# Kernel tuning notes

Measured on AMD Instinct MI355X. Metric: run time of the kernel, lower is better.

The kernel has to match this reference:

```python
import jax, jax.numpy as jnp
import numpy as np

EMBED_DIM = 1024
NUM_HEADS = 16
HEAD_DIM = EMBED_DIM // NUM_HEADS
CONSTANT = 1.0
EPS = 1e-4


def setup_inputs() -> dict:
    key = jax.random.key(0)
    ks = jax.random.split(key, 9)
    L, N, E = 2048, 4, EMBED_DIM
    scale = 1.0 / np.sqrt(E)
    return {
        "query": jax.random.normal(ks[0], (L, N, E), jnp.float32),
        "key": jax.random.normal(ks[1], (L, N, E), jnp.float32),
        "value": jax.random.normal(ks[2], (L, N, E), jnp.float32),
        "Wq": jax.random.normal(ks[3], (E, E), jnp.float32) * scale,
        "bq": jnp.zeros((E,), jnp.float32),
        "Wk": jax.random.normal(ks[4], (E, E), jnp.float32) * scale,
        "bk": jnp.zeros((E,), jnp.float32),
        "Wv": jax.random.normal(ks[5], (E, E), jnp.float32) * scale,
        "bv": jnp.zeros((E,), jnp.float32),
    }


def reference(query, key, value, Wq, bq, Wk, bk, Wv, bv):
    tgt_len, bsz, E = query.shape
    src_len = key.shape[0]
    h, d = NUM_HEADS, HEAD_DIM

    # Linear projections (nn.Linear: x @ W.T + b)
    q = query @ Wq.T + bq
    k = key @ Wk.T + bk
    v = value @ Wv.T + bv

    # (L, N, E) -> (N*h, L, d)
    def split_heads(x, slen):
        return x.reshape(slen, bsz * h, d).transpose(1, 0, 2)

    q = jax.nn.relu(split_heads(q, tgt_len))
    k = jax.nn.relu(split_heads(k, src_len))
    v = split_heads(v, src_len)

    # sin/cos positional reweighting: idx = pi/2 * arange(1, m+1) * constant / m
    m = max(src_len, tgt_len)
    idx = (np.pi / 2) * jnp.arange(1, m + 1, dtype=q.dtype) * CONSTANT / m  # (m,)
    sin_w = jnp.sin(idx)[None, :, None]  # (1, m, 1)
    cos_w = jnp.cos(idx)[None, :, None]

    q_ = jnp.concatenate([q * sin_w[:, :tgt_len], q * cos_w[:, :tgt_len]], axis=-1)  # (n, L, 2d)
    k_ = jnp.concatenate([k * sin_w[:, :src_len], k * cos_w[:, :src_len]], axis=-1)  # (n, S, 2d)

    # Non-causal linear attention: O(N) in sequence length
    kv_ = jnp.einsum('nld,nlm->ndm', k_, v)                       # (n, 2d, d)
    z_ = 1.0 / jnp.clip(jnp.einsum('nld,nd->nl', q_, k_.sum(axis=1)), EPS, None)  # (n, L)
    attn_output = jnp.einsum('nld,ndm,nl->nlm', q_, kv_, z_)      # (n, L, d)

    # (N*h, L, d) -> (L, N, E)
    attn_output = attn_output.transpose(1, 0, 2).reshape(tgt_len, bsz, E)
    return attn_output
```

## Files before the change

kernel.cpp:

```cpp
#include <hip/hip_runtime.h>
#include <cstdint>

#define L_SEQ 2048
#define NB 4
#define EMB 1024
#define NHEAD 16
#define HD 64
#define M_ROWS (L_SEQ * NB)
#define ANGC (1.5707963267948966f / 2048.0f)
#define NSPLIT 16
#define XN ((size_t)M_ROWS * EMB)
#define WN ((size_t)EMB * EMB)
#define NX8 (1 << 20)
#define NW8 (1 << 17)

typedef __bf16 bf16x8 __attribute__((ext_vector_type(8)));
typedef float f32x4 __attribute__((ext_vector_type(4)));
typedef unsigned short u16x8 __attribute__((ext_vector_type(8)));

__device__ __forceinline__ unsigned short f2bf(float f) {
  unsigned int u = __float_as_uint(f);
  u += 0x7fffu + ((u >> 16) & 1u);
  return (unsigned short)(u >> 16);
}
__device__ __forceinline__ float bf2f(unsigned short u) {
  return __uint_as_float((unsigned int)u << 16);
}

__device__ __forceinline__ void gload_lds16(const void* g, void* l) {
  __builtin_amdgcn_global_load_lds(
      (const __attribute__((address_space(1))) void*)g,
      (__attribute__((address_space(3))) void*)l, 16, 0, 0);
}

__global__ __launch_bounds__(256) void cvt_all_kernel(
    const float* __restrict__ q, const float* __restrict__ k,
    const float* __restrict__ v, const float* __restrict__ wq,
    const float* __restrict__ wk, const float* __restrict__ wv,
    unsigned short* __restrict__ xb, unsigned short* __restrict__ wb) {
  int i = blockIdx.x * 256 + threadIdx.x;
  const float* src;
  unsigned short* dst;
  int off;
  if (i < 3 * NX8) {
    int sel = i >> 20;
    off = i & (NX8 - 1);
    src = (sel == 0) ? q : (sel == 1) ? k : v;
    dst = xb + (size_t)sel * XN;
  } else {
    int j = i - 3 * NX8;
    int sel = j >> 17;
    off = j & (NW8 - 1);
    src = (sel == 0) ? wq : (sel == 1) ? wk : wv;
    dst = wb + (size_t)sel * WN;
  }
  const float4* s4 = (const float4*)src;
  float4 a = s4[off * 2], b = s4[off * 2 + 1];
  union { unsigned short u[8]; uint4 vv; } o;
  o.u[0] = f2bf(a.x); o.u[1] = f2bf(a.y); o.u[2] = f2bf(a.z); o.u[3] = f2bf(a.w);
  o.u[4] = f2bf(b.x); o.u[5] = f2bf(b.y); o.u[6] = f2bf(b.z); o.u[7] = f2bf(b.w);
  *(uint4*)(dst + (size_t)off * 8) = o.vv;
}

__global__ __launch_bounds__(256) void proj_gemm_kernel(
    const unsigned short* __restrict__ Xall, const unsigned short* __restrict__ Wall,
    const float* __restrict__ b0, const float* __restrict__ b1,
    const float* __restrict__ b2, unsigned short* __restrict__ Pall) {
  const int which = blockIdx.z;
  const unsigned short* Xb = Xall + (size_t)which * XN;
  const unsigned short* Wb = Wall + (size_t)which * WN;
  const float* bias = (which == 0) ? b0 : (which == 1) ? b1 : b2;
  unsigned short* outp = Pall + (size_t)which * XN;
  const bool relu = (which < 2);
  const int bm0 = blockIdx.x * 128;
  const int bn0 = blockIdx.y * 128;

  __shared__ unsigned short As[2][128 * 32];
  __shared__ unsigned short Bs[2][128 * 32];

  const int tid = threadIdx.x;
  const int lane = tid & 63, wave = tid >> 6;
  const int wrow = (wave >> 1) * 64, wcol = (wave & 1) * 64;
  const int fr = lane & 15, fk = lane >> 4;

  f32x4 acc[4][4];
#pragma unroll
  for (int m = 0; m < 4; ++m)
#pragma unroll
    for (int n = 0; n < 4; ++n) acc[m][n] = (f32x4){0.f, 0.f, 0.f, 0.f};

  auto stage = [&](int kt, int buf) {
#pragma unroll
    for (int i = 0; i < 2; ++i) {
      int c = i * 256 + wave * 64 + lane;
      int row = c >> 2;
      int kgs = (c & 3) ^ ((row >> 1) & 3);
      int ldsoff = (i * 256 + wave * 64) * 16;
      gload_lds16(Xb + (size_t)(bm0 + row) * EMB + kt * 32 + kgs * 8,
                  (char*)&As[buf][0] + ldsoff);
      gload_lds16(Wb + (size_t)(bn0 + row) * EMB + kt * 32 + kgs * 8,
                  (char*)&Bs[buf][0] + ldsoff);
    }
  };

  stage(0, 0);
  __syncthreads();
  const int NK = EMB / 32;
  for (int kt = 0; kt < NK; ++kt) {
    int buf = kt & 1;
    if (kt + 1 < NK) stage(kt + 1, buf ^ 1);
    bf16x8 af[4], bfr[4];
#pragma unroll
    for (int m = 0; m < 4; ++m) {
      int row = wrow + m * 16 + fr;
      af[m] = *(const bf16x8*)((const char*)&As[buf][0] + row * 64 +
                               ((fk ^ ((row >> 1) & 3)) * 16));
    }
#pragma unroll
    for (int n = 0; n < 4; ++n) {
      int row = wcol + n * 16 + fr;
      bfr[n] = *(const bf16x8*)((const char*)&Bs[buf][0] + row * 64 +
                                ((fk ^ ((row >> 1) & 3)) * 16));
    }
#pragma unroll
    for (int m = 0; m < 4; ++m)
#pragma unroll
      for (int n = 0; n < 4; ++n)
        acc[m][n] = __builtin_amdgcn_mfma_f32_16x16x32_bf16(af[m], bfr[n],
                                                            acc[m][n], 0, 0, 0);
    __syncthreads();
  }

#pragma unroll
  for (int n = 0; n < 4; ++n) {
    int gc = bn0 + wcol + n * 16 + fr;
    float bv = bias[gc];
#pragma unroll
    for (int m = 0; m < 4; ++m) {
#pragma unroll
      for (int r = 0; r < 4; ++r) {
        int gr = bm0 + wrow + m * 16 + fk * 4 + r;
        float v = acc[m][n][r] + bv;
        if (relu) v = fmaxf(v, 0.f);
        outp[(size_t)gr * EMB + gc] = f2bf(v);
      }
    }
  }
}

__global__ __launch_bounds__(256) void kv_part_kernel(
    const unsigned short* __restrict__ kp, const unsigned short* __restrict__ vp,
    float* __restrict__ kvpart, float* __restrict__ kspart) {
  const int n = blockIdx.y;
  const int s = blockIdx.x;
  const int nb = n >> 4, head = n & 15;
  const int l0 = s * (L_SEQ / NSPLIT);
  __shared__ float kt[32][64];
  __shared__ float vt[32][64];
  __shared__ float wt[2][32];
  const int t = threadIdx.x;
  const int dg = t >> 3, mg = t & 7;

  float acc[4][8];
#pragma unroll
  for (int a = 0; a < 4; ++a)
#pragma unroll
    for (int b = 0; b < 8; ++b) acc[a][b] = 0.f;
  float ks[4] = {0.f, 0.f, 0.f, 0.f};

  for (int lt = l0; lt < l0 + (L_SEQ / NSPLIT); lt += 32) {
    {
      int i = t >> 3, c8 = (t & 7) * 8;
      u16x8 gk8 = *(const u16x8*)(kp + (size_t)((lt + i) * NB + nb) * EMB +
                                  head * HD + c8);
      u16x8 gv8 = *(const u16x8*)(vp + (size_t)((lt + i) * NB + nb) * EMB +
                                  head * HD + c8);
      float4 ka = {bf2f(gk8[0]), bf2f(gk8[1]), bf2f(gk8[2]), bf2f(gk8[3])};
      float4 kb = {bf2f(gk8[4]), bf2f(gk8[5]), bf2f(gk8[6]), bf2f(gk8[7])};
      float4 va = {bf2f(gv8[0]), bf2f(gv8[1]), bf2f(gv8[2]), bf2f(gv8[3])};
      float4 vb = {bf2f(gv8[4]), bf2f(gv8[5]), bf2f(gv8[6]), bf2f(gv8[7])};
      *(float4*)&kt[i][c8] = ka;
      *(float4*)&kt[i][c8 + 4] = kb;
      *(float4*)&vt[i][c8] = va;
      *(float4*)&vt[i][c8 + 4] = vb;
    }
    if (t < 32) {
      float ang = ANGC * (float)(lt + t + 1);
      wt[0][t] = __sinf(ang);
      wt[1][t] = __cosf(ang);
    }
    __syncthreads();
#pragma unroll 4
    for (int i = 0; i < 32; ++i) {
      float w = wt[dg >> 4][i];
      float4 kk4 = *(const float4*)&kt[i][(dg & 15) * 4];
      float kk[4];
      kk[0] = fmaxf(kk4.x, 0.f) * w; kk[1] = fmaxf(kk4.y, 0.f) * w;
      kk[2] = fmaxf(kk4.z, 0.f) * w; kk[3] = fmaxf(kk4.w, 0.f) * w;
      float4 v0 = *(const float4*)&vt[i][mg * 8];
      float4 v1 = *(const float4*)&vt[i][mg * 8 + 4];
      float vv[8] = {v0.x, v0.y, v0.z, v0.w, v1.x, v1.y, v1.z, v1.w};
#pragma unroll
      for (int a = 0; a < 4; ++a) {
#pragma unroll
        for (int b = 0; b < 8; ++b) acc[a][b] += kk[a] * vv[b];
        ks[a] += kk[a];
      }
    }
    __syncthreads();
  }

  float* kvn = kvpart + ((size_t)(s * 64 + n) * 128 + dg * 4) * 64 + mg * 8;
#pragma unroll
  for (int a = 0; a < 4; ++a) {
    *(float4*)&kvn[(size_t)a * 64 + 0] = *(float4*)&acc[a][0];
    *(float4*)&kvn[(size_t)a * 64 + 4] = *(float4*)&acc[a][4];
  }
  if (mg == 0) {
#pragma unroll
    for (int a = 0; a < 4; ++a)
      kspart[(size_t)(s * 64 + n) * 128 + dg * 4 + a] = ks[a];
  }
}

__global__ __launch_bounds__(256) void kv_reduce_kernel(
    const float* __restrict__ kvpart, const float* __restrict__ kspart,
    float* __restrict__ kv, float* __restrict__ ksum) {
  const int b = blockIdx.x;
  const int t = threadIdx.x;
  if (b < 512) {
    int idx = b * 256 + t;
    f32x4 sum = (f32x4){0, 0, 0, 0};
#pragma unroll
    for (int p = 0; p < NSPLIT; ++p)
      sum += ((const f32x4*)kvpart)[(size_t)p * 131072 + idx];
    ((f32x4*)kv)[idx] = sum;
  } else {
#pragma unroll
    for (int j = 0; j < 8; ++j) {
      int idx = j * 256 + t;
      f32x4 sum = (f32x4){0, 0, 0, 0};
#pragma unroll
      for (int p = 0; p < NSPLIT; ++p)
        sum += ((const f32x4*)kspart)[(size_t)p * 2048 + idx];
      ((f32x4*)ksum)[idx] = sum;
    }
  }
}

__global__ __launch_bounds__(256) void out_kernel(
    const unsigned short* __restrict__ qp, const float* __restrict__ kv,
    const float* __restrict__ ksum, float* __restrict__ out) {
  const int n = blockIdx.y;
  const int nb = n >> 4, head = n & 15;
  const int L0 = blockIdx.x * 64;
  __shared__ float kvt[128][64];
  __shared__ float qt[64][68];
  __shared__ float kss[128];
  const int t = threadIdx.x;

  {
    const float4* src = (const float4*)(kv + (size_t)n * 128 * 64);
    float4* dst = (float4*)&kvt[0][0];
#pragma unroll
    for (int j = 0; j < 8; ++j) dst[j * 256 + t] = src[j * 256 + t];
    if (t < 128) kss[t] = ksum[n * 128 + t];
  }
  {
    int j = t >> 2, c16 = (t & 3) * 16;
    const unsigned short* gq =
        qp + (size_t)((L0 + j) * NB + nb) * EMB + head * HD + c16;
    u16x8 qa = *(const u16x8*)gq;
    u16x8 qb = *(const u16x8*)(gq + 8);
#pragma unroll
    for (int u = 0; u < 8; ++u) {
      qt[j][c16 + u] = fmaxf(bf2f(qa[u]), 0.f);
      qt[j][c16 + 8 + u] = fmaxf(bf2f(qb[u]), 0.f);
    }
  }
  __syncthreads();

  const int lg = t >> 4, mg = t & 15;
  float sw[4], cw[4];
#pragma unroll
  for (int a = 0; a < 4; ++a) {
    float ang = ANGC * (float)(L0 + lg * 4 + a + 1);
    sw[a] = __sinf(ang);
    cw[a] = __cosf(ang);
  }

  f32x4 accs[4], accc[4];
  float dns[4] = {0, 0, 0, 0}, dnc[4] = {0, 0, 0, 0};
#pragma unroll
  for (int a = 0; a < 4; ++a) {
    accs[a] = (f32x4){0, 0, 0, 0};
    accc[a] = (f32x4){0, 0, 0, 0};
  }

#pragma unroll 4
  for (int c = 0; c < 64; ++c) {
    f32x4 kvs = *(const f32x4*)&kvt[c][mg * 4];
    f32x4 kvc = *(const f32x4*)&kvt[64 + c][mg * 4];
    float kssv = kss[c], kscv = kss[64 + c];
#pragma unroll
    for (int a = 0; a < 4; ++a) {
      float qv = qt[lg * 4 + a][c];
      accs[a] += qv * kvs;
      accc[a] += qv * kvc;
      dns[a] += qv * kssv;
      dnc[a] += qv * kscv;
    }
  }

#pragma unroll
  for (int a = 0; a < 4; ++a) {
    float den = sw[a] * dns[a] + cw[a] * dnc[a];
    float z = 1.f / fmaxf(den, 1e-4f);
    int l = L0 + lg * 4 + a;
    f32x4 o = (sw[a] * accs[a] + cw[a] * accc[a]) * z;
    *(f32x4*)&out[((size_t)l * NB + nb) * EMB + head * HD + mg * 4] = o;
  }
}

extern "C" void kernel_launch(void* const* d_in, const int* in_sizes, int n_in,
                              void* d_out, int out_size, void* d_ws, size_t ws_size,
                              hipStream_t stream) {
  const float* query = (const float*)d_in[0];
  const float* key = (const float*)d_in[1];
  const float* value = (const float*)d_in[2];
  const float* Wq = (const float*)d_in[3];
  const float* bq = (const float*)d_in[4];
  const float* Wk = (const float*)d_in[5];
  const float* bk = (const float*)d_in[6];
  const float* Wv = (const float*)d_in[7];
  const float* bv = (const float*)d_in[8];
  float* out = (float*)d_out;

  char* ws = (char*)d_ws;
  const size_t need = 3 * XN * 2 + 3 * WN * 2 + 3 * XN * 2 +
                      (size_t)(64 * 128 * 64 + 64 * 128) * 4;
  if (ws_size < need) return;

  unsigned short* xb = (unsigned short*)ws;
  unsigned short* wb = (unsigned short*)(ws + 3 * XN * 2);
  unsigned short* proj = (unsigned short*)(ws + 3 * XN * 2 + 3 * WN * 2);
  float* kvb = (float*)(ws + 3 * XN * 2 + 3 * WN * 2 + 3 * XN * 2);
  float* ksb = kvb + 64 * 128 * 64;
  float* kvpart = (float*)ws;
  float* kspart = (float*)(ws + (size_t)NSPLIT * 64 * 128 * 64 * 4);

  const int total8 = 3 * NX8 + 3 * NW8;
  cvt_all_kernel<<<total8 / 256, 256, 0, stream>>>(query, key, value, Wq, Wk, Wv,
                                                   xb, wb);
  proj_gemm_kernel<<<dim3(64, 8, 3), 256, 0, stream>>>(xb, wb, bq, bk, bv, proj);
  kv_part_kernel<<<dim3(NSPLIT, 64), 256, 0, stream>>>(proj + 1 * XN, proj + 2 * XN,
                                                       kvpart, kspart);
  kv_reduce_kernel<<<513, 256, 0, stream>>>(kvpart, kspart, kvb, ksb);
  out_kernel<<<dim3(32, 64), 256, 0, stream>>>(proj, kvb, ksb, out);
}
```

Baseline: 344.2 us.

## Compute attention output with bf16 MFMA and emit transposed bf16 KV from reduce

The output stage now folds the sin/cos weights into a bf16 copy of q in LDS and runs the q·kv product on MFMA 16x16x32 bf16 instructions in place of scalar fp32 FMAs. The normaliser is computed separately from LDS. The reduce kernel now makes one block per head, sums the partial kv results, and writes kv transposed as bf16 to suit the MFMA B operand. The projection GEMM is split into three templated launches, one per matrix, with the branch on which matrix is selected at compile time. Rounding q·sin/cos and kv to bf16 lowers accuracy, the reduce step now runs on only 64 blocks, and the three separate GEMM launches add launch overhead.

```diff
diff --git a/kernel.cpp b/kernel.cpp
--- a/kernel.cpp
+++ b/kernel.cpp
@@ -62,16 +62,14 @@
   *(uint4*)(dst + (size_t)off * 8) = o.vv;
 }
 
+template <int WHICH>
 __global__ __launch_bounds__(256) void proj_gemm_kernel(
     const unsigned short* __restrict__ Xall, const unsigned short* __restrict__ Wall,
-    const float* __restrict__ b0, const float* __restrict__ b1,
-    const float* __restrict__ b2, unsigned short* __restrict__ Pall) {
-  const int which = blockIdx.z;
-  const unsigned short* Xb = Xall + (size_t)which * XN;
-  const unsigned short* Wb = Wall + (size_t)which * WN;
-  const float* bias = (which == 0) ? b0 : (which == 1) ? b1 : b2;
-  unsigned short* outp = Pall + (size_t)which * XN;
-  const bool relu = (which < 2);
+    const float* __restrict__ bias, unsigned short* __restrict__ Pall) {
+  const unsigned short* Xb = Xall + (size_t)WHICH * XN;
+  const unsigned short* Wb = Wall + (size_t)WHICH * WN;
+  unsigned short* outp = Pall + (size_t)WHICH * XN;
+  const bool relu = (WHICH < 2);
   const int bm0 = blockIdx.x * 128;
   const int bn0 = blockIdx.y * 128;
 
@@ -225,100 +223,135 @@
 
 __global__ __launch_bounds__(256) void kv_reduce_kernel(
     const float* __restrict__ kvpart, const float* __restrict__ kspart,
-    float* __restrict__ kv, float* __restrict__ ksum) {
-  const int b = blockIdx.x;
+    unsigned short* __restrict__ kvT, float* __restrict__ ksum) {
+  const int n = blockIdx.x;
   const int t = threadIdx.x;
-  if (b < 512) {
-    int idx = b * 256 + t;
-    f32x4 sum = (f32x4){0, 0, 0, 0};
+  __shared__ float kvsum[128][65];
+
+#pragma unroll
+  for (int j = 0; j < 8; ++j) {
+    int f4 = j * 256 + t;
+    int dd = f4 >> 4, m4 = f4 & 15;
+    f32x4 s = (f32x4){0, 0, 0, 0};
 #pragma unroll
     for (int p = 0; p < NSPLIT; ++p)
-      sum += ((const f32x4*)kvpart)[(size_t)p * 131072 + idx];
-    ((f32x4*)kv)[idx] = sum;
-  } else {
-#pragma unroll
-    for (int j = 0; j < 8; ++j) {
-      int idx = j * 256 + t;
-      f32x4 sum = (f32x4){0, 0, 0, 0};
-#pragma unroll
-      for (int p = 0; p < NSPLIT; ++p)
-        sum += ((const f32x4*)kspart)[(size_t)p * 2048 + idx];
-      ((f32x4*)ksum)[idx] = sum;
-    }
-  }
-}
-
-__global__ __launch_bounds__(256) void out_kernel(
-    const unsigned short* __restrict__ qp, const float* __restrict__ kv,
+      s += *(const f32x4*)(kvpart + (((size_t)(p * 64 + n) * 128 + dd) * 64) +
+                           m4 * 4);
+    kvsum[dd][m4 * 4 + 0] = s[0];
+    kvsum[dd][m4 * 4 + 1] = s[1];
+    kvsum[dd][m4 * 4 + 2] = s[2];
+    kvsum[dd][m4 * 4 + 3] = s[3];
+  }
+  if (t < 128) {
+    float s = 0.f;
+#pragma unroll
+    for (int p = 0; p < NSPLIT; ++p) s += kspart[(size_t)(p * 64 + n) * 128 + t];
+    ksum[n * 128 + t] = s;
+  }
+  __syncthreads();
+
+  int m = t >> 2, dseg = t & 3;
+#pragma unroll
+  for (int gg = 0; gg < 4; ++gg) {
+    int dd0 = dseg * 32 + gg * 8;
+    union { unsigned short u[8]; uint4 vv; } o;
+#pragma unroll
+    for (int e = 0; e < 8; ++e) o.u[e] = f2bf(kvsum[dd0 + e][m]);
+    *(uint4*)(kvT + ((size_t)n * 64 + m) * 128 + dd0) = o.vv;
+  }
+}
+
+__global__ __launch_bounds__(256) void out_mfma_kernel(
+    const unsigned short* __restrict__ qp, const unsigned short* __restrict__ kvT,
     const float* __restrict__ ksum, float* __restrict__ out) {
   const int n = blockIdx.y;
   const int nb = n >> 4, head = n & 15;
   const int L0 = blockIdx.x * 64;
-  __shared__ float kvt[128][64];
-  __shared__ float qt[64][68];
-  __shared__ float kss[128];
   const int t = threadIdx.x;
+  const int lane = t & 63, wave = t >> 6;
+  const int fr = lane & 15, fk = lane >> 4;
+
+  __shared__ unsigned short q_lds[64 * 128];
+  __shared__ unsigned short kvt_lds[64 * 128];
+  __shared__ float ks_lds[128];
+  __shared__ float z_lds[64];
 
   {
-    const float4* src = (const float4*)(kv + (size_t)n * 128 * 64);
-    float4* dst = (float4*)&kvt[0][0];
-#pragma unroll
-    for (int j = 0; j < 8; ++j) dst[j * 256 + t] = src[j * 256 + t];
-    if (t < 128) kss[t] = ksum[n * 128 + t];
-  }
-  {
-    int j = t >> 2, c16 = (t & 3) * 16;
+    int j = t >> 2, d0 = (t & 3) * 16;
+    float ang = ANGC * (float)(L0 + j + 1);
+    float sw = __sinf(ang), cw = __cosf(ang);
     const unsigned short* gq =
-        qp + (size_t)((L0 + j) * NB + nb) * EMB + head * HD + c16;
+        qp + (size_t)((L0 + j) * NB + nb) * EMB + head * HD + d0;
     u16x8 qa = *(const u16x8*)gq;
     u16x8 qb = *(const u16x8*)(gq + 8);
-#pragma unroll
-    for (int u = 0; u < 8; ++u) {
-      qt[j][c16 + u] = fmaxf(bf2f(qa[u]), 0.f);
-      qt[j][c16 + 8 + u] = fmaxf(bf2f(qb[u]), 0.f);
-    }
-  }
+    union { unsigned short u[8]; uint4 vv; } s0, s1, c0, c1;
+#pragma unroll
+    for (int e = 0; e < 8; ++e) {
+      float fa = fmaxf(bf2f(qa[e]), 0.f);
+      float fb = fmaxf(bf2f(qb[e]), 0.f);
+      s0.u[e] = f2bf(fa * sw); s1.u[e] = f2bf(fb * sw);
+      c0.u[e] = f2bf(fa * cw); c1.u[e] = f2bf(fb * cw);
+    }
+    int gs = (t & 3) * 2;
+    *(uint4*)&q_lds[(j * 16 + ((gs + 0) ^ (j & 7))) * 8] = s0.vv;
+    *(uint4*)&q_lds[(j * 16 + ((gs + 1) ^ (j & 7))) * 8] = s1.vv;
+    *(uint4*)&q_lds[(j * 16 + ((gs + 8) ^ (j & 7))) * 8] = c0.vv;
+    *(uint4*)&q_lds[(j * 16 + ((gs + 9) ^ (j & 7))) * 8] = c1.vv;
+  }
+  {
+#pragma unroll
+    for (int c = 0; c < 4; ++c) {
+      int gi = t * 4 + c;
+      int m = gi >> 4, g = gi & 15;
+      uint4 v = *(const uint4*)(kvT + (size_t)n * 8192 + m * 128 + g * 8);
+      *(uint4*)&kvt_lds[(m * 16 + (g ^ (m & 7))) * 8] = v;
+    }
+  }
+  if (t < 128) ks_lds[t] = ksum[n * 128 + t];
   __syncthreads();
 
-  const int lg = t >> 4, mg = t & 15;
-  float sw[4], cw[4];
-#pragma unroll
-  for (int a = 0; a < 4; ++a) {
-    float ang = ANGC * (float)(L0 + lg * 4 + a + 1);
-    sw[a] = __sinf(ang);
-    cw[a] = __cosf(ang);
-  }
-
-  f32x4 accs[4], accc[4];
-  float dns[4] = {0, 0, 0, 0}, dnc[4] = {0, 0, 0, 0};
-#pragma unroll
-  for (int a = 0; a < 4; ++a) {
-    accs[a] = (f32x4){0, 0, 0, 0};
-    accc[a] = (f32x4){0, 0, 0, 0};
-  }
-
-#pragma unroll 4
-  for (int c = 0; c < 64; ++c) {
-    f32x4 kvs = *(const f32x4*)&kvt[c][mg * 4];
-    f32x4 kvc = *(const f32x4*)&kvt[64 + c][mg * 4];
-    float kssv = kss[c], kscv = kss[64 + c];
-#pragma unroll
-    for (int a = 0; a < 4; ++a) {
-      float qv = qt[lg * 4 + a][c];
-      accs[a] += qv * kvs;
-      accc[a] += qv * kvc;
-      dns[a] += qv * kssv;
-      dnc[a] += qv * kscv;
-    }
-  }
-
-#pragma unroll
-  for (int a = 0; a < 4; ++a) {
-    float den = sw[a] * dns[a] + cw[a] * dnc[a];
-    float z = 1.f / fmaxf(den, 1e-4f);
-    int l = L0 + lg * 4 + a;
-    f32x4 o = (sw[a] * accs[a] + cw[a] * accc[a]) * z;
-    *(f32x4*)&out[((size_t)l * NB + nb) * EMB + head * HD + mg * 4] = o;
+  {
+    int row = t >> 2, seg = t & 3;
+    float sum = 0.f;
+#pragma unroll
+    for (int g8 = 0; g8 < 4; ++g8) {
+      int g = seg * 4 + g8;
+      const unsigned short* qg = &q_lds[(row * 16 + (g ^ (row & 7))) * 8];
+      u16x8 qv = *(const u16x8*)qg;
+#pragma unroll
+      for (int e = 0; e < 8; ++e) sum += bf2f(qv[e]) * ks_lds[g * 8 + e];
+    }
+    sum += __shfl_xor(sum, 1);
+    sum += __shfl_xor(sum, 2);
+    if (seg == 0) z_lds[row] = 1.f / fmaxf(sum, 1e-4f);
+  }
+
+  const int wrow = wave * 16;
+  f32x4 acc[4];
+#pragma unroll
+  for (int nt = 0; nt < 4; ++nt) acc[nt] = (f32x4){0, 0, 0, 0};
+#pragma unroll
+  for (int kk = 0; kk < 4; ++kk) {
+    int arow = wrow + fr;
+    bf16x8 af = *(const bf16x8*)&q_lds[(arow * 16 + ((kk * 4 + fk) ^ (arow & 7))) * 8];
+#pragma unroll
+    for (int nt = 0; nt < 4; ++nt) {
+      int brow = nt * 16 + fr;
+      bf16x8 bf =
+          *(const bf16x8*)&kvt_lds[(brow * 16 + ((kk * 4 + fk) ^ (brow & 7))) * 8];
+      acc[nt] = __builtin_amdgcn_mfma_f32_16x16x32_bf16(af, bf, acc[nt], 0, 0, 0);
+    }
+  }
+
+#pragma unroll
+  for (int nt = 0; nt < 4; ++nt) {
+#pragma unroll
+    for (int r = 0; r < 4; ++r) {
+      int lrow = wrow + fk * 4 + r;
+      int m = nt * 16 + fr;
+      out[((size_t)(L0 + lrow) * NB + nb) * EMB + head * HD + m] =
+          acc[nt][r] * z_lds[lrow];
+    }
   }
 }
 
@@ -338,23 +371,26 @@
 
   char* ws = (char*)d_ws;
   const size_t need = 3 * XN * 2 + 3 * WN * 2 + 3 * XN * 2 +
-                      (size_t)(64 * 128 * 64 + 64 * 128) * 4;
+                      (size_t)64 * 64 * 128 * 2 + (size_t)64 * 128 * 4;
   if (ws_size < need) return;
 
   unsigned short* xb = (unsigned short*)ws;
   unsigned short* wb = (unsigned short*)(ws + 3 * XN * 2);
   unsigned short* proj = (unsigned short*)(ws + 3 * XN * 2 + 3 * WN * 2);
-  float* kvb = (float*)(ws + 3 * XN * 2 + 3 * WN * 2 + 3 * XN * 2);
-  float* ksb = kvb + 64 * 128 * 64;
+  unsigned short* kvT = (unsigned short*)(ws + 3 * XN * 2 + 3 * WN * 2 + 3 * XN * 2);
+  float* ksb = (float*)(ws + 3 * XN * 2 + 3 * WN * 2 + 3 * XN * 2 +
+                        (size_t)64 * 64 * 128 * 2);
   float* kvpart = (float*)ws;
   float* kspart = (float*)(ws + (size_t)NSPLIT * 64 * 128 * 64 * 4);
 
   const int total8 = 3 * NX8 + 3 * NW8;
   cvt_all_kernel<<<total8 / 256, 256, 0, stream>>>(query, key, value, Wq, Wk, Wv,
                                                    xb, wb);
-  proj_gemm_kernel<<<dim3(64, 8, 3), 256, 0, stream>>>(xb, wb, bq, bk, bv, proj);
+  proj_gemm_kernel<0><<<dim3(64, 8), 256, 0, stream>>>(xb, wb, bq, proj);
+  proj_gemm_kernel<1><<<dim3(64, 8), 256, 0, stream>>>(xb, wb, bk, proj);
+  proj_gemm_kernel<2><<<dim3(64, 8), 256, 0, stream>>>(xb, wb, bv, proj);
   kv_part_kernel<<<dim3(NSPLIT, 64), 256, 0, stream>>>(proj + 1 * XN, proj + 2 * XN,
                                                        kvpart, kspart);
-  kv_reduce_kernel<<<513, 256, 0, stream>>>(kvpart, kspart, kvb, ksb);
-  out_kernel<<<dim3(32, 64), 256, 0, stream>>>(proj, kvb, ksb, out);
-}
+  kv_reduce_kernel<<<64, 256, 0, stream>>>(kvpart, kspart, kvT, ksb);
+  out_mfma_kernel<<<dim3(32, 64), 256, 0, stream>>>(proj, kvT, ksb, out);
+}
```

Result: faster. 301.1 us (-12.5%).
